# Performance work log

Hardware: AMD Instinct MI355X
Metric: run time of the kernel (lower is better)

Reference implementation:

```python
import jax, jax.numpy as jnp
import numpy as np
from jax import lax

IMG = 1280.0          # image side (80 * stride 16)
HF = WF = 80          # feature map
STRIDE = 16
A = 15                # anchors per location (5 sizes x 3 ratios)
KMIX = 5              # MDN mixture components
NIMG = 8
NGT = 32
PRE_NMS = 2000
POST_NMS = 1000
NMS_THRESH = 0.7
BATCH_PER_IMG = 256
POS_FRAC = 0.5
SCALE_CLAMP = float(np.log(1000.0 / 16.0))
LOG2PI = float(np.log(2.0 * np.pi))


def _make_anchors():
    sizes = np.array([32., 64., 128., 256., 512.])
    ratios = np.array([0.5, 1.0, 2.0])
    ws = (sizes[:, None] * np.sqrt(1.0 / ratios)[None, :]).reshape(-1)
    hs = (sizes[:, None] * np.sqrt(ratios)[None, :]).reshape(-1)
    base = np.stack([-ws / 2, -hs / 2, ws / 2, hs / 2], 1)  # [A,4]
    xs = (np.arange(WF) + 0.5) * STRIDE
    ys = (np.arange(HF) + 0.5) * STRIDE
    sx, sy = np.meshgrid(xs, ys)
    shifts = np.stack([sx.ravel(), sy.ravel(), sx.ravel(), sy.ravel()], 1)  # [HW,4]
    return jnp.asarray((shifts[:, None, :] + base[None]).reshape(-1, 4), jnp.float32)


def setup_inputs() -> dict:
    key = jax.random.key(0)
    k = jax.random.split(key, 6)
    R = HF * WF * A
    anchors = _make_anchors()                                                # [R,4]
    pi = jax.random.normal(k[0], (NIMG, KMIX, R), jnp.float32)
    mu = jax.random.normal(k[1], (NIMG, KMIX, R), jnp.float32)
    sigma = jax.random.uniform(k[2], (NIMG, KMIX, R), jnp.float32, 0.1, 1.0)
    deltas = jax.random.normal(k[3], (NIMG, R, 4), jnp.float32) * 0.1
    xy = jax.random.uniform(k[4], (NIMG, NGT, 2), jnp.float32, 0.0, 960.0)
    wh = jax.random.uniform(k[5], (NIMG, NGT, 2), jnp.float32, 20.0, 320.0)
    gt_boxes = jnp.concatenate([xy, xy + wh], -1)                            # [N,G,4]
    return {"anchors": anchors, "pi": pi, "mu": mu, "sigma": sigma,
            "deltas": deltas, "gt_boxes": gt_boxes}


def pairwise_iou(a, b):  # [M,4],[P,4] -> [M,P]
    area_a = (a[:, 2] - a[:, 0]) * (a[:, 3] - a[:, 1])
    area_b = (b[:, 2] - b[:, 0]) * (b[:, 3] - b[:, 1])
    lt = jnp.maximum(a[:, None, :2], b[None, :, :2])
    rb = jnp.minimum(a[:, None, 2:], b[None, :, 2:])
    wh = jnp.clip(rb - lt, 0.0)
    inter = wh[..., 0] * wh[..., 1]
    return inter / jnp.maximum(area_a[:, None] + area_b[None, :] - inter, 1e-9)


def apply_deltas(d, boxes):  # Box2BoxTransform.apply_deltas, weights=(1,1,1,1)
    w = boxes[:, 2] - boxes[:, 0]
    h = boxes[:, 3] - boxes[:, 1]
    cx = boxes[:, 0] + 0.5 * w
    cy = boxes[:, 1] + 0.5 * h
    dx, dy = d[:, 0], d[:, 1]
    dw = jnp.minimum(d[:, 2], SCALE_CLAMP)
    dh = jnp.minimum(d[:, 3], SCALE_CLAMP)
    pcx = dx * w + cx
    pcy = dy * h + cy
    pw = jnp.exp(dw) * w
    ph = jnp.exp(dh) * h
    return jnp.stack([pcx - 0.5 * pw, pcy - 0.5 * ph, pcx + 0.5 * pw, pcy + 0.5 * ph], 1)


def get_deltas(src, tgt):  # Box2BoxTransform.get_deltas
    sw = src[..., 2] - src[..., 0]
    sh = src[..., 3] - src[..., 1]
    scx = src[..., 0] + 0.5 * sw
    scy = src[..., 1] + 0.5 * sh
    tw = tgt[..., 2] - tgt[..., 0]
    th = tgt[..., 3] - tgt[..., 1]
    tcx = tgt[..., 0] + 0.5 * tw
    tcy = tgt[..., 1] + 0.5 * th
    return jnp.stack([(tcx - scx) / sw, (tcy - scy) / sh,
                      jnp.log(tw / sw), jnp.log(th / sh)], -1)


def _nms_image(boxes, scores, unc):  # [R,4],[R],[R,2] -> padded top proposals
    top_s, tidx = lax.top_k(scores, PRE_NMS)
    tb = jnp.clip(boxes[tidx], 0.0, IMG)   # clip to image
    tu = unc[tidx]
    iou = pairwise_iou(tb, tb)             # [PRE,PRE]
    ar = jnp.arange(PRE_NMS)

    def body(i, keep):
        sup = (iou[i] > NMS_THRESH) & (ar > i) & keep[i]
        return keep & ~sup

    keep = lax.fori_loop(0, PRE_NMS, body, jnp.ones((PRE_NMS,), bool))
    wv = tb[:, 2] - tb[:, 0]
    hv = tb[:, 3] - tb[:, 1]
    keep = keep & (wv > 0.0) & (hv > 0.0)  # min_box_size = 0
    ms = jnp.where(keep, top_s, -jnp.inf)
    out_s, oidx = lax.top_k(ms, POST_NMS)
    return tb[oidx], out_s, tu[oidx]


def _losses(anchors, pi, mu, sigma, deltas, gt_boxes):
    # label_and_sample_anchors (no_grad in torch)
    iou = lax.stop_gradient(jax.vmap(lambda g: pairwise_iou(g, anchors))(gt_boxes))  # [N,G,R]
    vals = iou.max(axis=1)                       # matched IoU quality  [N,R]
    idx = jnp.argmax(iou, axis=1)                # matched gt index     [N,R]
    labels = jnp.where(vals >= 0.7, 1, jnp.where(vals >= 0.3, -1, 0))
    best_gt = iou.max(axis=2)                    # [N,G]
    lq = jnp.any((iou >= best_gt[:, :, None] - 1e-7) & (best_gt[:, :, None] > 0), axis=1)
    labels = jnp.where(lq, 1, labels)            # allow_low_quality_matches
    # deterministic subsample to batch_size_per_image with positive_fraction
    pos = labels == 1
    neg = labels == 0
    n_pos = jnp.minimum(pos.sum(1), int(BATCH_PER_IMG * POS_FRAC))
    keep_pos = pos & (jnp.cumsum(pos, 1) <= n_pos[:, None])
    keep_neg = neg & (jnp.cumsum(neg, 1) <= (BATCH_PER_IMG - n_pos)[:, None])
    labels = jnp.where(keep_pos, 1, jnp.where(keep_neg, 0, -1))
    matched_gt = lax.stop_gradient(jax.vmap(lambda g, i: g[i])(gt_boxes, idx))  # [N,R,4]
    gt_deltas = get_deltas(lax.stop_gradient(anchors)[None], matched_gt)
    pos_mask = labels == 1
    # smooth_l1 with beta=0 -> L1, summed over positives
    loss_loc = jnp.sum(jnp.abs(deltas - gt_deltas) * pos_mask[..., None])
    valid = labels != -1
    t = jnp.clip(vals, 0.0, 1.0)
    lp = jax.nn.log_softmax(pi, axis=1)
    comp = lp - 0.5 * ((t[:, None, :] - mu) / sigma) ** 2 - jnp.log(sigma) - 0.5 * LOG2PI
    nll = -jax.nn.logsumexp(comp, axis=1)        # [N,R]
    loss_cls = jnp.sum(nll * valid)
    norm = BATCH_PER_IMG * pi.shape[0]
    return jnp.stack([loss_cls / norm, loss_loc / norm])


def reference(anchors, pi, mu, sigma, deltas, gt_boxes):
    # find_logit: pi-weighted mixture mean as objectness score
    pi_sm = jax.nn.softmax(pi, axis=1)           # [N,K,R]
    logits = jnp.sum(pi_sm * mu, axis=1)         # [N,R]
    # mdn_uncertainties: epistemic / aleatoric
    epis = jnp.sum(pi_sm * (mu - logits[:, None, :]) ** 2, axis=1)
    alea = jnp.sum(pi_sm * sigma ** 2, axis=1)
    unc = jnp.stack([epis, alea], -1)            # [N,R,2]
    # _decode_proposals
    boxes = jax.vmap(lambda d: apply_deltas(d, anchors))(deltas)  # [N,R,4]
    # find_top_rpn_proposals_uncertainty (pre-NMS topk, clip, NMS, post-NMS topk)
    prop_b, prop_s, prop_u = jax.vmap(_nms_image)(boxes, logits, unc)
    losses = _losses(anchors, pi, mu, sigma, deltas, gt_boxes)    # [loss_cls, loss_loc]
    return prop_b, prop_s, prop_u, losses
```

## Files before the change

### kernel.cpp

```cpp
#include <hip/hip_runtime.h>
#include <cstdint>
#include <cstddef>

typedef unsigned long long u64;
typedef unsigned int u32;
typedef unsigned short u16;
typedef unsigned char u8;

#define R_ANCH 96000
#define R4     24000
#define NIMG   8
#define KMIX   5
#define PRE    2000
#define POST   1000
#define NGT    32
#define NCHUNK 375
#define ACHUNK 94
#define NBLK   48
#define MROW   2048
#define SCAP   16
#define BIG_TH 64
#define CAP_BIN 6144
#define CAND_CAP 8192
#define GC_STRIDE 16
#define RPART  32

#define IMG_SZ        1280.0f
#define NMS_T         0.7f
#define SCALE_CLAMP_F 4.135166556742356f
#define HALF_L2PI     0.9189385332046727f

__device__ __forceinline__ u64 make_key(float s, int r) {
  u32 u = __float_as_uint(s);
  u = (u & 0x80000000u) ? ~u : (u | 0x80000000u);
  return ((u64)u << 32) | (u64)(0xFFFFFFFFu - (u32)r);
}

__device__ __forceinline__ float dec_score(u64 key) {
  u32 o = (u32)(key >> 32);
  u32 bits = (o & 0x80000000u) ? (o ^ 0x80000000u) : ~o;
  return __uint_as_float(bits);
}

__device__ __forceinline__ float iou_pair(float a0,float a1,float a2,float a3,
                                          float b0,float b1,float b2,float b3) {
#pragma clang fp contract(off)
  float areaA = (a2-a0)*(a3-a1);
  float areaB = (b2-b0)*(b3-b1);
  float lx=fmaxf(a0,b0), ly=fmaxf(a1,b1);
  float rx=fminf(a2,b2), ry=fminf(a3,b3);
  float iw=fmaxf(rx-lx,0.0f), ih=fmaxf(ry-ly,0.0f);
  float inter=iw*ih;
  return inter / fmaxf(areaA+areaB-inter, 1e-9f);
}

// ... 197 lines not shown
    int r = bx*256 + tid;
    if (tid < NGT*4) s_gt[tid] = gt[img*NGT*4 + tid];
    if (tid < NGT){
      const float* g4 = gt + img*NGT*4 + tid*4;
      s_ga[tid] = (g4[2]-g4[0])*(g4[3]-g4[1]);
      s_bg[tid] = __int_as_float(best[img*NGT + tid]);
    }
    __syncthreads();
    float4 a = ((const float4*)anchors)[r];
    float aA = (a.z-a.x)*(a.w-a.y);
    float bi=-1.0f, bu=1.0f; bool lq = false;
#pragma unroll 4
    for (int g=0; g<NGT; ++g){
      float g0=s_gt[g*4], g1=s_gt[g*4+1], g2=s_gt[g*4+2], g3=s_gt[g*4+3];
      float lx=fmaxf(g0,a.x), ly=fmaxf(g1,a.y);
      float rx=fminf(g2,a.z), ry=fminf(g3,a.w);
      float iw=fmaxf(rx-lx,0.0f), ih=fmaxf(ry-ly,0.0f);
      float inter=iw*ih;
      float uni = fmaxf(s_ga[g] + aA - inter, 1e-9f);
      if (inter*bu > bi*uni){ bi=inter; bu=uni; }
      float bg = s_bg[g];
      lq = lq || ((inter >= (bg - 1e-7f)*uni) && (bg > 0.0f));
    }
    float vbest = bi/bu;
    int lab = lq ? 1 : (vbest >= 0.7f ? 1 : (vbest >= 0.3f ? -1 : 0));
    label[(size_t)img*R_ANCH + r] = (signed char)lab;
    u64 bp = __ballot(lab==1), bn = __ballot(lab==0);
    int wid = tid>>6, lane = tid&63;
    if (lane==0){ s_w[wid*2]=__popcll(bp); s_w[wid*2+1]=__popcll(bn); }
    __syncthreads();
    if (tid==0){
      cpos[img*NCHUNK + bx] = s_w[0]+s_w[2]+s_w[4]+s_w[6];
      cneg[img*NCHUNK + bx] = s_w[1]+s_w[3]+s_w[5]+s_w[7];
    }
    return;
  }

  __shared__ u32 s_h[2048];
  __shared__ int s_i[8]; __shared__ u32 s_u[3];
  int d0,k0; u32 c0;
  pick2048(hist0 + img*2048, PRE, s_i, s_u, d0,k0,c0);
  if (c0 <= CAP_BIN) return;
  for (int b=tid; b<2048; b+=256) s_h[b]=0u;
  __syncthreads();
  const float* sc = logits + (size_t)img*R_ANCH;
  for (int r = blockIdx.x*256 + tid; r < R_ANCH; r += NBLK*256){
    u64 key = make_key(sc[r], r);
    if ((int)(key>>53) == d0) atomicAdd(&s_h[(u32)(key>>42)&2047u], 1u);
  }
  __syncthreads();
  for (int b=tid; b<2048; b+=256){ u32 v=s_h[b]; if(v) atomicAdd(&hist1[img*2048+b], v); }
}

__global__ __launch_bounds__(256) void kP2(const float* __restrict__ logits,
                                           const u32* __restrict__ hist0,
                                           const u32* __restrict__ hist1,
                                           u32* __restrict__ hist2) {
  __shared__ u32 s_h[2048];
  __shared__ int s_i[8]; __shared__ u32 s_u[3];
  int img = blockIdx.y, tid = threadIdx.x;
  int d0,k0; u32 c0;
  pick2048(hist0 + img*2048, PRE, s_i, s_u, d0,k0,c0);
  if (c0 <= CAP_BIN) return;
  int d1,k1; u32 c1;
  pick2048(hist1 + img*2048, k0, s_i, s_u, d1,k1,c1);
  if (c1 <= CAP_BIN) return;
  u64 p1 = ((u64)d0<<11) | (u64)d1;
  for (int b=tid; b<2048; b+=256) s_h[b]=0u;
  __syncthreads();
  const float* sc = logits + (size_t)img*R_ANCH;
  for (int r = blockIdx.x*256 + tid; r < R_ANCH; r += NBLK*256){
    u64 key = make_key(sc[r], r);
    if ((key>>42) == p1) atomicAdd(&s_h[(u32)(key>>31)&2047u], 1u);
  }
  __syncthreads();
  for (int b=tid; b<2048; b+=256){ u32 v=s_h[b]; if(v) atomicAdd(&hist2[img*2048+b], v); }
}

__global__ __launch_bounds__(256) void kGatherL4(const float* __restrict__ logits,
    const u32* __restrict__ hist0, const u32* __restrict__ hist1,
    const u32* __restrict__ hist2, u64* __restrict__ cand, u32* __restrict__ gcnt,
    const signed char* __restrict__ label,
    const float* __restrict__ pi, const float* __restrict__ mu,
    const float* __restrict__ sigma, const float* __restrict__ anchors,
    const float* __restrict__ gt, const float* __restrict__ deltas,
    const int* __restrict__ cpos, const int* __restrict__ cneg,
    float* __restrict__ acc) {
  int img = blockIdx.y, tid = threadIdx.x;

  if (blockIdx.x >= NBLK) {
    __shared__ int s_wp[4], s_wn[4];
    __shared__ int s_r[12];
    __shared__ float s_red[8];
    __shared__ float s_gt[NGT*4];
    int bx = blockIdx.x - NBLK;
    int lane = tid & 63, wid = tid >> 6;
    if (tid < NGT*4) s_gt[tid] = gt[img*NGT*4 + tid];
    int vp=0, vn=0, tp=0;
    for (int k=tid; k<NCHUNK; k+=256){
      int cp = cpos[img*NCHUNK + k];
      int cn = cneg[img*NCHUNK + k];
      tp += cp;
      if (k < bx){ vp += cp; vn += cn; }
    }
    for (int of=32; of>0; of>>=1){
      vp += __shfl_down(vp, of, 64);
      vn += __shfl_down(vn, of, 64);
      tp += __shfl_down(tp, of, 64);
    }
    if (lane==0){ s_r[wid]=vp; s_r[4+wid]=vn; s_r[8+wid]=tp; }
    __syncthreads();
    int pre_p = s_r[0]+s_r[1]+s_r[2]+s_r[3];
    int pre_n = s_r[4]+s_r[5]+s_r[6]+s_r[7];
    int totp  = s_r[8]+s_r[9]+s_r[10]+s_r[11];
    int np = totp < 128 ? totp : 128;
    int nn = 256 - np;
    int r = bx*256 + tid;
    size_t o = (size_t)img*R_ANCH + r;
    int lab = label[o];
    bool pos = (lab==1), neg = (lab==0);
    u64 bp = __ballot(pos), bn = __ballot(neg);
    if (lane==0){ s_wp[wid]=__popcll(bp); s_wn[wid]=__popcll(bn); }
    __syncthreads();
    for (int w=0; w<wid; ++w){ pre_p += s_wp[w]; pre_n += s_wn[w]; }
    u64 lm = (1ull<<lane) - 1ull;
    pre_p += __popcll(bp & lm);
    pre_n += __popcll(bn & lm);
    bool kp = pos && (pre_p < np);
    bool kn = neg && (pre_n < nn);
    float c_cls = 0.0f, c_loc = 0.0f;
    if (kp || kn){
      float4 a = ((const float4*)anchors)[r];
      float aA = (a.z-a.x)*(a.w-a.y);
      float bi = -1.0f, bu = 1.0f; int idx = 0;
// ... 16 lines not shown
        p[k]=pi[base+(size_t)k*R_ANCH];
        m[k]=mu[base+(size_t)k*R_ANCH];
        s[k]=sigma[base+(size_t)k*R_ANCH];
      }
      float mx = p[0];
#pragma unroll
      for (int k=1;k<KMIX;k++) mx = fmaxf(mx,p[k]);
      float e[KMIX]; float sum = 0.0f;
#pragma unroll
      for (int k=0;k<KMIX;k++){ e[k]=expf(p[k]-mx); sum += e[k]; }
      float lsum = logf(sum);
      float t_ = fminf(fmaxf(vbest, 0.0f), 1.0f);
      float comp[KMIX];
#pragma unroll
      for (int k=0;k<KMIX;k++){
        float z = (t_ - m[k]) / s[k];
        comp[k] = (p[k]-mx-lsum) - 0.5f*z*z - logf(s[k]) - HALF_L2PI;
      }
      float cm = comp[0];
#pragma unroll
      for (int k=1;k<KMIX;k++) cm = fmaxf(cm, comp[k]);
      float se = 0.0f;
#pragma unroll
      for (int k=0;k<KMIX;k++) se += expf(comp[k]-cm);
      c_cls = -(cm + logf(se));
      if (kp){
        const float* gb = &s_gt[idx*4];
        float sw = a.z-a.x, sh = a.w-a.y;
        float scx = a.x+0.5f*sw, scy = a.y+0.5f*sh;
        float tw = gb[2]-gb[0], th = gb[3]-gb[1];
        float tcx = gb[0]+0.5f*tw, tcy = gb[1]+0.5f*th;
        float4 d = ((const float4*)deltas)[(size_t)img*R_ANCH + r];
        c_loc = fabsf(d.x-(tcx-scx)/sw) + fabsf(d.y-(tcy-scy)/sh)
              + fabsf(d.z-logf(tw/sw)) + fabsf(d.w-logf(th/sh));
      }
    }
    for (int of=32; of>0; of>>=1){
      c_cls += __shfl_down(c_cls, of, 64);
      c_loc += __shfl_down(c_loc, of, 64);
    }
    if (lane==0){ s_red[wid]=c_cls; s_red[4+wid]=c_loc; }
    __syncthreads();
    if (tid==0){
      float a = s_red[0]+s_red[1]+s_red[2]+s_red[3];
      float b = s_red[4]+s_red[5]+s_red[6]+s_red[7];
      if (a != 0.0f) atomicAdd(&acc[0], a);
      if (b != 0.0f) atomicAdd(&acc[1], b);
    }
    return;
  }

  __shared__ int s_i[8]; __shared__ u32 s_u[3];
  __shared__ u64 s_cand[2048];
  __shared__ u32 s_cnt, s_base;
  if (tid==0) s_cnt = 0u;
  int d,kk; u32 c;
  pick2048(hist0 + img*2048, PRE, s_i, s_u, d,kk,c);
  u64 p = (u64)d; int L = 0;
  if (c > CAP_BIN){
    pick2048(hist1 + img*2048, kk, s_i, s_u, d,kk,c);
    p = (p<<11)|(u64)d; L = 1;
    if (c > CAP_BIN){
      pick2048(hist2 + img*2048, kk, s_i, s_u, d,kk,c);
      p = (p<<11)|(u64)d; L = 2;
    }
  }
  u64 T = p << (64 - 11*(L+1));
  const float* sc = logits + (size_t)img*R_ANCH;
  int lane = tid & 63;
  for (int r = blockIdx.x*256 + tid; r < R_ANCH; r += NBLK*256){
    u64 key = make_key(sc[r], r);
    bool take = (key >= T);
    u64 b = __ballot(take);
    if (b){
      u32 base = 0;
      if (lane==0) base = atomicAdd(&s_cnt, (u32)__popcll(b));
      base = (u32)__shfl((int)base, 0, 64);
      if (take){
        u32 pos = base + (u32)__popcll(b & ((1ull<<lane)-1ull));
        if (pos < 2048u) s_cand[pos] = key;
        else {
          u32 gp = atomicAdd(&gcnt[img*GC_STRIDE], 1u);
          if (gp < CAND_CAP) cand[(size_t)img*CAND_CAP + gp] = key;
        }
      }
    }
  }
  __syncthreads();
  u32 n = s_cnt < 2048u ? s_cnt : 2048u;
  if (tid==0) s_base = atomicAdd(&gcnt[img*GC_STRIDE], n);
  __syncthreads();
  u32 gb = s_base;
  for (u32 i=tid; i<n; i+=256)
    cand[(size_t)img*CAND_CAP + gb + i] = s_cand[i];
}

__global__ __launch_bounds__(1024) void kRank(
    const u64* __restrict__ cand, const u32* __restrict__ gcnt,
    const float* __restrict__ epis, const float* __restrict__ alea,
    const float* __restrict__ deltas, const float* __restrict__ anchors,
    float* __restrict__ tb, float* __restrict__ tu, float* __restrict__ ts) {
  __shared__ u64 s_key[CAND_CAP];
  __shared__ u16 s_idx0[CAND_CAP];
  __shared__ u16 s_idx1[CAND_CAP];
  __shared__ u32 s_h0[2048];
  __shared__ u32 s_off0[2048];
  __shared__ u32 s_h1[2048];
  __shared__ u32 s_off1[2048];
  __shared__ u32 s_wsum[16];
  __shared__ u32 s_nbig;
  __shared__ u16 s_big[128];
  int tid = threadIdx.x, part = blockIdx.x, img = blockIdx.y;
  u32 cnt = gcnt[img*GC_STRIDE];
  if (cnt > (u32)CAND_CAP) cnt = CAND_CAP;
  const u64* cp = cand + (size_t)img*CAND_CAP;
  for (int i=tid; i<CAND_CAP; i+=1024) s_key[i] = (i < (int)cnt) ? cp[i] : 0ull;
  for (int b=tid; b<2048; b+=1024){ s_h0[b] = 0u; }
  if (tid==0) s_nbig = 0u;
  __syncthreads();
  for (int i=tid; i<(int)cnt; i+=1024)
    atomicAdd(&s_h0[(u32)(s_key[i]>>53)], 1u);
  __syncthreads();
  scan2048_desc(s_h0, s_off0, s_wsum, tid);
  __syncthreads();
  for (int b=tid; b<2048; b+=1024){
    u32 sz = s_h0[b];
    if (sz > BIG_TH && s_off0[b] < PRE && (b % RPART) == part){
      u32 q = atomicAdd(&s_nbig, 1u);
      if (q < 128u) s_big[q] = (u16)b;
    }
  }
  __syncthreads();
  for (int i=tid; i<(int)cnt; i+=1024){
    u32 d = (u32)(s_key[i]>>53);
    u32 slot = atomicAdd(&s_off0[d], 1u);
    s_idx0[slot] = (u16)i;
  }
  __syncthreads();
  auto emit = [&](u64 my, u32 rank){
    if (rank < PRE){
      int p = (int)rank;
      u32 idx = 0xFFFFFFFFu - (u32)(my & 0xFFFFFFFFull);
      ts[img*PRE + p] = dec_score(my);
      float4 a = ((const float4*)anchors)[idx];
      float4 dd = ((const float4*)deltas)[(size_t)img*R_ANCH + idx];
      float w = a.z - a.x, h = a.w - a.y;
      float cx = a.x + 0.5f*w, cy = a.y + 0.5f*h;
      float dw = fminf(dd.z, SCALE_CLAMP_F), dh = fminf(dd.w, SCALE_CLAMP_F);
      float pcx = dd.x*w + cx, pcy = dd.y*h + cy;
      float pw = expf(dw)*w, ph = expf(dh)*h;
      float x0 = fminf(fmaxf(pcx - 0.5f*pw, 0.0f), IMG_SZ);
      float y0 = fminf(fmaxf(pcy - 0.5f*ph, 0.0f), IMG_SZ);
      float x1 = fminf(fmaxf(pcx + 0.5f*pw, 0.0f), IMG_SZ);
      float y1 = fminf(fmaxf(pcy + 0.5f*ph, 0.0f), IMG_SZ);
      ((float4*)tb)[(size_t)img*PRE + p] = make_float4(x0,y0,x1,y1);
      size_t o = (size_t)img*R_ANCH + idx;
      ((float2*)tu)[(size_t)img*PRE + p] = make_float2(epis[o], alea[o]);
    }
  };
  {
    int lo = (int)(((long long)cnt * part) / RPART);
    int hi = (int)(((long long)cnt * (part+1)) / RPART);
    for (int i=lo+tid; i<hi; i+=1024){
      u64 my = s_key[i];
      u32 d = (u32)(my>>53);
      u32 size = s_h0[d];
      if (size > BIG_TH) continue;
      u32 bs = s_off0[d] - size;
      if (bs >= PRE) continue;
      u32 rank = bs;
      for (u32 q=bs; q<bs+size; ++q)
        rank += (s_key[s_idx0[q]] > my) ? 1u : 0u;
      emit(my, rank);
    }
  }
  __syncthreads();
  u32 nbig = s_nbig < 128u ? s_nbig : 128u;
  for (u32 bb=0; bb<nbig; ++bb){
    u32 B = s_big[bb];
    u32 size = s_h0[B];
    u32 base0 = s_off0[B] - size;
    for (int b=tid; b<2048; b+=1024) s_h1[b] = 0u;
    __syncthreads();
    for (u32 q=tid; q<size; q+=1024){
      u64 k = s_key[s_idx0[base0+q]];
      atomicAdd(&s_h1[(u32)(k>>42)&2047u], 1u);
    }
    __syncthreads();
    scan2048_desc(s_h1, s_off1, s_wsum, tid);
    __syncthreads();
    for (u32 q=tid; q<size; q+=1024){
      u16 ci = s_idx0[base0+q];
      u64 k = s_key[ci];
      u32 slot = atomicAdd(&s_off1[(u32)(k>>42)&2047u], 1u);
      s_idx1[slot] = ci;
    }
    __syncthreads();
    for (u32 q=tid; q<size; q+=1024){
      u16 ci = s_idx1[q];
      u64 my = s_key[ci];
      u32 d1 = (u32)(my>>42)&2047u;
      u32 ssz = s_h1[d1];
      u32 sbs = s_off1[d1] - ssz;
      u32 rank = base0 + sbs;
      for (u32 t2=sbs; t2<sbs+ssz; ++t2)
        rank += (s_key[s_idx1[t2]] > my) ? 1u : 0u;
      emit(my, rank);
    }
    __syncthreads();
  }
}

__global__ __launch_bounds__(1024) void kD_mask(const float* __restrict__ tb,
                                                u64* __restrict__ maskLT,
                                                u32* __restrict__ scnt,
                                                u16* __restrict__ slist) {
  __shared__ float4 s_tile[64];
  int tid = threadIdx.x;
  int a = blockIdx.x, img = blockIdx.y;
  const float4* tbi = (const float4*)tb + (size_t)img*PRE;
  if (tid < 64){
    int i = a*64 + tid;
    s_tile[tid] = (i < PRE) ? tbi[i] : make_float4(0.f,0.f,0.f,0.f);
  }
  __syncthreads();
  u64* outp = maskLT + ((size_t)img*32 + a)*MROW;
  u32* cnts = scnt + (size_t)img*2048;
  u16* lst  = slist + (size_t)img*2048*SCAP;
  int bmax = min(64, PRE - a*64);
  for (int j = a*64 + tid; j < MROW; j += 1024){
    u64 m = 0ull;
    if (j < PRE){
      float4 B = tbi[j];
      int blim = min(bmax, j - a*64);
      for (int b = 0; b < blim; ++b){
        float4 A = s_tile[b];
        float v = iou_pair(A.x,A.y,A.z,A.w, B.x,B.y,B.z,B.w);
        m |= (u64)(v > NMS_T) << b;
      }
    }
    outp[j] = m;
    u64 mm = m;
    while (mm){
      int b = __builtin_ctzll(mm); mm &= mm - 1ull;
      u32 slot = atomicAdd(&cnts[j], 1u);
      if (slot < SCAP) lst[(size_t)j*SCAP + slot] = (u16)(a*64 + b);
    }
  }
}

__global__ __launch_bounds__(1024) void kEF_nms(const u64* __restrict__ maskLT,
    const u32* __restrict__ scnt, const u16* __restrict__ slist,
    const float* __restrict__ tb, const float* __restrict__ tu,
    const float* __restrict__ ts, const float* __restrict__ acc,
    float* __restrict__ out) {
  __shared__ u64 s_list64[2048*SCAP/4];
  __shared__ u16 s_cnt[2048];
  __shared__ u8  kbuf[2][2048];
  __shared__ u64 s_kw[32];
  __shared__ int s_change, s_ovf;
  __shared__ int s_wk[16], s_wn[16];
  __shared__ int s_kc, s_runk, s_runn;
  int img = blockIdx.x, tid = threadIdx.x;
  int lane = tid & 63, wid = tid >> 6;
  const u64* gl = (const u64*)(slist + (size_t)img*2048*SCAP);
  for (int i=tid; i<2048*SCAP/4; i+=1024) s_list64[i] = gl[i];
  const u32* gc = scnt + (size_t)img*2048;
  for (int i=tid; i<2048; i+=1024) s_cnt[i] = (u16)gc[i];
  if (tid==0){ s_change = 0; s_ovf = 0; }
  __syncthreads();
  bool myovf = false;
#pragma unroll
  for (int q=0; q<2; ++q){
    int j = tid + q*1024;
    if (s_cnt[j] > SCAP) myovf = true;
    kbuf[0][j] = (j < PRE) ? 1 : 0;
  }
  if (myovf) s_ovf = 1;
  __syncthreads();
  const u64* MT = maskLT + (size_t)img*32*MROW;
  int cur = 0;
  for (int iter=0; iter<2048; ++iter){
    bool ovf = (s_ovf != 0);
    if (ovf && tid < 32){
      u64 w = 0ull;
      for (int b=0; b<64; ++b) w |= (u64)(kbuf[cur][tid*64+b] & 1) << b;
      s_kw[tid] = w;
    }
    __syncthreads();
    bool changed = false;
#pragma unroll
    for (int q=0; q<2; ++q){
      int j = tid + q*1024;
      u8 old = kbuf[cur][j];
      u8 nk = (j < PRE) ? 1 : 0;
      if (nk){
        int cnt = s_cnt[j];
        if (cnt <= SCAP){
          const u16* lp = (const u16*)&s_list64[j*(SCAP/4)];
          for (int i=0; i<cnt; ++i){
            if (kbuf[cur][lp[i]]){ nk = 0; break; }
          }
        } else {
          int amax = j >> 6;
          for (int a=0; a<=amax; ++a){
            if (MT[(size_t)a*MROW + j] & s_kw[a]){ nk = 0; break; }
          }
        }
      }
      kbuf[1-cur][j] = nk;
      changed |= (nk != old);
    }
    if (changed) s_change = 1;
    __syncthreads();
    int ch = s_change;
    __syncthreads();
    if (tid==0) s_change = 0;
    if (!ch) break;
    cur ^= 1;
  }
  __syncthreads();
  const float4* tbi = (const float4*)tb + (size_t)img*PRE;
  const float NEG_INF = __uint_as_float(0xff800000u);
  u8* kf = kbuf[1-cur];
#pragma unroll
  for (int cch=0; cch<2; ++cch){
    int pp = cch*1024 + tid;
    bool kp = false;
    if (pp < PRE && kbuf[cur][pp]){
      float4 b = tbi[pp];
      kp = (b.z > b.x) && (b.w > b.y);
    }
    kf[pp] = kp ? 1 : 0;
  }
  __syncthreads();
  {
    int cc = (int)kf[tid] + (int)kf[1024 + tid];
    for (int of=32; of>0; of>>=1) cc += __shfl_down(cc, of, 64);
    if (lane==0) s_wk[wid] = cc;
  }
  __syncthreads();
  if (tid==0){
    int t=0; for (int w=0; w<16; ++w) t += s_wk[w];
    s_kc = t; s_runk = 0; s_runn = 0;
  }
  __syncthreads();
  int kc = s_kc;
#pragma unroll
  for (int cch=0; cch<2; ++cch){
    int pp = cch*1024 + tid;
    bool kp = kf[pp] != 0;
    u64 bk = __ballot(kp), bn = __ballot(!kp);
    if (lane==0){ s_wk[wid]=__popcll(bk); s_wn[wid]=__popcll(bn); }
    __syncthreads();
    int pk = s_runk, pn = s_runn;
    for (int w=0; w<wid; ++w){ pk += s_wk[w]; pn += s_wn[w]; }
    u64 lm = (1ull<<lane) - 1ull;
    pk += __popcll(bk & lm);
    pn += __popcll(bn & lm);
    int slot = kp ? pk : (kc + pn);
    if (slot < POST && pp < PRE){
      ((float4*)out)[img*POST + slot] = tbi[pp];
      out[32000 + img*POST + slot] = kp ? ts[img*PRE + pp] : NEG_INF;
      ((float2*)(out + 40000))[img*POST + slot] = ((const float2*)tu)[(size_t)img*PRE + pp];
    }
    __syncthreads();
    if (tid==0){
      int tk=0, tn=0;
      for (int w=0; w<16; ++w){ tk += s_wk[w]; tn += s_wn[w]; }
      s_runk += tk; s_runn += tn;
    }
    __syncthreads();
  }
  if (img==0 && tid<2) out[56000+tid] = acc[tid] * (1.0f/2048.0f);
}

extern "C" void kernel_launch(void* const* d_in, const int* in_sizes, int n_in,
                              void* d_out, int out_size, void* d_ws, size_t ws_size,
                              hipStream_t stream) {
  const float* anchors = (const float*)d_in[0];
  const float* pi      = (const float*)d_in[1];
  const float* mu      = (const float*)d_in[2];
  const float* sigma   = (const float*)d_in[3];
  const float* deltas  = (const float*)d_in[4];
  const float* gt      = (const float*)d_in[5];
  float* out = (float*)d_out;

  char* ws = (char*)d_ws;
  size_t off = 0;
  auto alloc = [&](size_t bytes) -> void* {
    void* p = (void*)(ws + off);
    off += (bytes + 255) & ~(size_t)255;
    return p;
  };
  float* logits = (float*)alloc((size_t)NIMG*R_ANCH*4);
  float* epis   = (float*)alloc((size_t)NIMG*R_ANCH*4);
  float* alea   = (float*)alloc((size_t)NIMG*R_ANCH*4);
  signed char* label = (signed char*)alloc((size_t)NIMG*R_ANCH);
  float* tb     = (float*)alloc((size_t)NIMG*PRE*4*4);
  float* tu     = (float*)alloc((size_t)NIMG*PRE*2*4);
  float* ts     = (float*)alloc((size_t)NIMG*PRE*4);
  u64*   maskLT = (u64*)  alloc((size_t)NIMG*32*MROW*8);
  u16*   slist  = (u16*)  alloc((size_t)NIMG*2048*SCAP*2);
  u64*   cand   = (u64*)  alloc((size_t)NIMG*CAND_CAP*8);
  int*   cpos   = (int*)  alloc((size_t)NIMG*NCHUNK*4);
  int*   cneg   = (int*)  alloc((size_t)NIMG*NCHUNK*4);
  size_t zstart = off;
  u32*   hist0  = (u32*)  alloc((size_t)NIMG*2048*4);
  u32*   hist1  = (u32*)  alloc((size_t)NIMG*2048*4);
  u32*   hist2  = (u32*)  alloc((size_t)NIMG*2048*4);
  u32*   gcnt   = (u32*)  alloc((size_t)NIMG*GC_STRIDE*4);
  int*   best   = (int*)  alloc((size_t)NIMG*NGT*4);
  u32*   scnt   = (u32*)  alloc((size_t)NIMG*2048*4);
  float* acc    = (float*)alloc(8);
  int zwords = (int)((off - zstart) / 4);

  kZero<<<dim3(64), dim3(256), 0, stream>>>((u32*)(ws + zstart), zwords);
  kA_mdn<<<dim3(ACHUNK+NBLK, NIMG), dim3(256), 0, stream>>>(pi, mu, sigma, logits, epis, alea,
                                                            hist0, anchors, gt, best);
  kP1L2<<<dim3(NBLK+NCHUNK, NIMG), dim3(256), 0, stream>>>(logits, hist0, hist1,
                                                           anchors, gt, best, label, cpos, cneg);
  kP2<<<dim3(NBLK, NIMG), dim3(256), 0, stream>>>(logits, hist0, hist1, hist2);
  kGatherL4<<<dim3(NBLK+NCHUNK, NIMG), dim3(256), 0, stream>>>(logits, hist0, hist1, hist2,
                                                               cand, gcnt, label, pi, mu, sigma,
                                                               anchors, gt, deltas, cpos, cneg, acc);
  kRank<<<dim3(RPART, NIMG), dim3(1024), 0, stream>>>(cand, gcnt, epis, alea, deltas, anchors, tb, tu, ts);
  kD_mask<<<dim3(32, NIMG), dim3(1024), 0, stream>>>(tb, maskLT, scnt, slist);
  kEF_nms<<<dim3(NIMG), dim3(1024), 0, stream>>>(maskLT, scnt, slist, tb, tu, ts, acc, out);
}
```

Before: 239.3 us.

## Fuse rank, NMS-mask and NMS kernels into one cooperative kernel; drop kP2

Rank, IoU-mask build and NMS selection now run in one cooperatively launched kernel. Phases are separated by grid-wide syncs, and shared memory is reused through a union. The separate level-2 histogram kernel is removed: when a third radix level is needed, each gather block builds that histogram redundantly in its own shared memory. This cuts two kernel launches and their inter-kernel gaps. In exchange it adds grid-sync cost, requires all blocks to be co-resident, and makes every gather block rescan the full logit array when the rare level-2 case triggers.

```diff
diff --git a/kernel.cpp b/kernel.cpp
--- a/kernel.cpp
+++ b/kernel.cpp
@@ -1,6 +1,9 @@
 #include <hip/hip_runtime.h>
+#include <hip/hip_cooperative_groups.h>
 #include <cstdint>
 #include <cstddef>
+
+namespace cg = cooperative_groups;
 
 typedef unsigned long long u64;
 typedef unsigned int u32;
@@ -304,34 +307,9 @@
   for (int b=tid; b<2048; b+=256){ u32 v=s_h[b]; if(v) atomicAdd(&hist1[img*2048+b], v); }
 }
 
-__global__ __launch_bounds__(256) void kP2(const float* __restrict__ logits,
-                                           const u32* __restrict__ hist0,
-                                           const u32* __restrict__ hist1,
-                                           u32* __restrict__ hist2) {
-  __shared__ u32 s_h[2048];
-  __shared__ int s_i[8]; __shared__ u32 s_u[3];
-  int img = blockIdx.y, tid = threadIdx.x;
-  int d0,k0; u32 c0;
-  pick2048(hist0 + img*2048, PRE, s_i, s_u, d0,k0,c0);
-  if (c0 <= CAP_BIN) return;
-  int d1,k1; u32 c1;
-  pick2048(hist1 + img*2048, k0, s_i, s_u, d1,k1,c1);
-  if (c1 <= CAP_BIN) return;
-  u64 p1 = ((u64)d0<<11) | (u64)d1;
-  for (int b=tid; b<2048; b+=256) s_h[b]=0u;
-  __syncthreads();
-  const float* sc = logits + (size_t)img*R_ANCH;
-  for (int r = blockIdx.x*256 + tid; r < R_ANCH; r += NBLK*256){
-    u64 key = make_key(sc[r], r);
-    if ((key>>42) == p1) atomicAdd(&s_h[(u32)(key>>31)&2047u], 1u);
-  }
-  __syncthreads();
-  for (int b=tid; b<2048; b+=256){ u32 v=s_h[b]; if(v) atomicAdd(&hist2[img*2048+b], v); }
-}
-
 __global__ __launch_bounds__(256) void kGatherL4(const float* __restrict__ logits,
     const u32* __restrict__ hist0, const u32* __restrict__ hist1,
-    const u32* __restrict__ hist2, u64* __restrict__ cand, u32* __restrict__ gcnt,
+    u64* __restrict__ cand, u32* __restrict__ gcnt,
     const signed char* __restrict__ label,
     const float* __restrict__ pi, const float* __restrict__ mu,
     const float* __restrict__ sigma, const float* __restrict__ anchors,
@@ -454,21 +432,29 @@
 
   __shared__ int s_i[8]; __shared__ u32 s_u[3];
   __shared__ u64 s_cand[2048];
+  __shared__ u32 s_h2[2048];
   __shared__ u32 s_cnt, s_base;
   if (tid==0) s_cnt = 0u;
   int d,kk; u32 c;
   pick2048(hist0 + img*2048, PRE, s_i, s_u, d,kk,c);
   u64 p = (u64)d; int L = 0;
+  const float* sc = logits + (size_t)img*R_ANCH;
   if (c > CAP_BIN){
     pick2048(hist1 + img*2048, kk, s_i, s_u, d,kk,c);
     p = (p<<11)|(u64)d; L = 1;
     if (c > CAP_BIN){
-      pick2048(hist2 + img*2048, kk, s_i, s_u, d,kk,c);
+      for (int b=tid; b<2048; b+=256) s_h2[b] = 0u;
+      __syncthreads();
+      for (int r = tid; r < R_ANCH; r += 256){
+        u64 key = make_key(sc[r], r);
+        if ((key>>42) == p) atomicAdd(&s_h2[(u32)(key>>31)&2047u], 1u);
+      }
+      __syncthreads();
+      pick2048(s_h2, kk, s_i, s_u, d,kk,c);
       p = (p<<11)|(u64)d; L = 2;
     }
   }
   u64 T = p << (64 - 11*(L+1));
-  const float* sc = logits + (size_t)img*R_ANCH;
   int lane = tid & 63;
   for (int r = blockIdx.x*256 + tid; r < R_ANCH; r += NBLK*256){
     u64 key = make_key(sc[r], r);
@@ -497,284 +483,293 @@
     cand[(size_t)img*CAND_CAP + gb + i] = s_cand[i];
 }
 
-__global__ __launch_bounds__(1024) void kRank(
+struct RankS {
+  u64 s_key[CAND_CAP];
+  u16 s_idx0[CAND_CAP];
+  u16 s_idx1[CAND_CAP];
+  u32 s_h0[2048];
+  u32 s_off0[2048];
+  u32 s_h1[2048];
+  u32 s_off1[2048];
+  u32 s_wsum[16];
+  u32 s_nbig;
+  u16 s_big[128];
+};
+struct DmaskS { float4 s_tile[64]; };
+struct EfS {
+  u64 s_list64[2048*SCAP/4];
+  u16 s_cnt[2048];
+  u8  kbuf[2][2048];
+  u64 s_kw[32];
+  int s_change, s_ovf;
+  int s_wk[16], s_wn[16];
+  int s_kc, s_runk, s_runn;
+};
+
+__global__ __launch_bounds__(1024) void kRDE(
     const u64* __restrict__ cand, const u32* __restrict__ gcnt,
     const float* __restrict__ epis, const float* __restrict__ alea,
     const float* __restrict__ deltas, const float* __restrict__ anchors,
-    float* __restrict__ tb, float* __restrict__ tu, float* __restrict__ ts) {
-  __shared__ u64 s_key[CAND_CAP];
-  __shared__ u16 s_idx0[CAND_CAP];
-  __shared__ u16 s_idx1[CAND_CAP];
-  __shared__ u32 s_h0[2048];
-  __shared__ u32 s_off0[2048];
-  __shared__ u32 s_h1[2048];
-  __shared__ u32 s_off1[2048];
-  __shared__ u32 s_wsum[16];
-  __shared__ u32 s_nbig;
-  __shared__ u16 s_big[128];
-  int tid = threadIdx.x, part = blockIdx.x, img = blockIdx.y;
-  u32 cnt = gcnt[img*GC_STRIDE];
-  if (cnt > (u32)CAND_CAP) cnt = CAND_CAP;
-  const u64* cp = cand + (size_t)img*CAND_CAP;
-  for (int i=tid; i<CAND_CAP; i+=1024) s_key[i] = (i < (int)cnt) ? cp[i] : 0ull;
-  for (int b=tid; b<2048; b+=1024){ s_h0[b] = 0u; }
-  if (tid==0) s_nbig = 0u;
-  __syncthreads();
-  for (int i=tid; i<(int)cnt; i+=1024)
-    atomicAdd(&s_h0[(u32)(s_key[i]>>53)], 1u);
-  __syncthreads();
-  scan2048_desc(s_h0, s_off0, s_wsum, tid);
-  __syncthreads();
-  for (int b=tid; b<2048; b+=1024){
-    u32 sz = s_h0[b];
-    if (sz > BIG_TH && s_off0[b] < PRE && (b % RPART) == part){
-      u32 q = atomicAdd(&s_nbig, 1u);
-      if (q < 128u) s_big[q] = (u16)b;
-    }
-  }
-  __syncthreads();
-  for (int i=tid; i<(int)cnt; i+=1024){
-    u32 d = (u32)(s_key[i]>>53);
-    u32 slot = atomicAdd(&s_off0[d], 1u);
-    s_idx0[slot] = (u16)i;
-  }
-  __syncthreads();
-  auto emit = [&](u64 my, u32 rank){
-    if (rank < PRE){
-      int p = (int)rank;
-      u32 idx = 0xFFFFFFFFu - (u32)(my & 0xFFFFFFFFull);
-      ts[img*PRE + p] = dec_score(my);
-      float4 a = ((const float4*)anchors)[idx];
-      float4 dd = ((const float4*)deltas)[(size_t)img*R_ANCH + idx];
-      float w = a.z - a.x, h = a.w - a.y;
-      float cx = a.x + 0.5f*w, cy = a.y + 0.5f*h;
-      float dw = fminf(dd.z, SCALE_CLAMP_F), dh = fminf(dd.w, SCALE_CLAMP_F);
-      float pcx = dd.x*w + cx, pcy = dd.y*h + cy;
-      float pw = expf(dw)*w, ph = expf(dh)*h;
-      float x0 = fminf(fmaxf(pcx - 0.5f*pw, 0.0f), IMG_SZ);
-      float y0 = fminf(fmaxf(pcy - 0.5f*ph, 0.0f), IMG_SZ);
-      float x1 = fminf(fmaxf(pcx + 0.5f*pw, 0.0f), IMG_SZ);
-      float y1 = fminf(fmaxf(pcy + 0.5f*ph, 0.0f), IMG_SZ);
-      ((float4*)tb)[(size_t)img*PRE + p] = make_float4(x0,y0,x1,y1);
-      size_t o = (size_t)img*R_ANCH + idx;
-      ((float2*)tu)[(size_t)img*PRE + p] = make_float2(epis[o], alea[o]);
-    }
-  };
+    float* __restrict__ tb, float* __restrict__ tu, float* __restrict__ ts,
+    u64* __restrict__ maskLT, u32* __restrict__ scnt, u16* __restrict__ slist,
+    const float* __restrict__ acc, float* __restrict__ out) {
+  __shared__ union { RankS r; DmaskS d; EfS e; } sm;
+  cg::grid_group grid = cg::this_grid();
+  int tid = threadIdx.x;
+  int gblk = blockIdx.x;
+
   {
-    int lo = (int)(((long long)cnt * part) / RPART);
-    int hi = (int)(((long long)cnt * (part+1)) / RPART);
-    for (int i=lo+tid; i<hi; i+=1024){
-      u64 my = s_key[i];
-      u32 d = (u32)(my>>53);
-      u32 size = s_h0[d];
-      if (size > BIG_TH) continue;
-      u32 bs = s_off0[d] - size;
-      if (bs >= PRE) continue;
-      u32 rank = bs;
-      for (u32 q=bs; q<bs+size; ++q)
-        rank += (s_key[s_idx0[q]] > my) ? 1u : 0u;
-      emit(my, rank);
-    }
-  }
-  __syncthreads();
-  u32 nbig = s_nbig < 128u ? s_nbig : 128u;
-  for (u32 bb=0; bb<nbig; ++bb){
-    u32 B = s_big[bb];
-    u32 size = s_h0[B];
-    u32 base0 = s_off0[B] - size;
-    for (int b=tid; b<2048; b+=1024) s_h1[b] = 0u;
-    __syncthreads();
-    for (u32 q=tid; q<size; q+=1024){
-      u64 k = s_key[s_idx0[base0+q]];
-      atomicAdd(&s_h1[(u32)(k>>42)&2047u], 1u);
-    }
-    __syncthreads();
-    scan2048_desc(s_h1, s_off1, s_wsum, tid);
-    __syncthreads();
-    for (u32 q=tid; q<size; q+=1024){
-      u16 ci = s_idx0[base0+q];
-      u64 k = s_key[ci];
-      u32 slot = atomicAdd(&s_off1[(u32)(k>>42)&2047u], 1u);
-      s_idx1[slot] = ci;
-    }
-    __syncthreads();
-    for (u32 q=tid; q<size; q+=1024){
-      u16 ci = s_idx1[q];
-      u64 my = s_key[ci];
-      u32 d1 = (u32)(my>>42)&2047u;
-      u32 ssz = s_h1[d1];
-      u32 sbs = s_off1[d1] - ssz;
-      u32 rank = base0 + sbs;
-      for (u32 t2=sbs; t2<sbs+ssz; ++t2)
-        rank += (s_key[s_idx1[t2]] > my) ? 1u : 0u;
-      emit(my, rank);
-    }
-    __syncthreads();
-  }
-}
-
-__global__ __launch_bounds__(1024) void kD_mask(const float* __restrict__ tb,
-                                                u64* __restrict__ maskLT,
-                                                u32* __restrict__ scnt,
-                                                u16* __restrict__ slist) {
-  __shared__ float4 s_tile[64];
-  int tid = threadIdx.x;
-  int a = blockIdx.x, img = blockIdx.y;
-  const float4* tbi = (const float4*)tb + (size_t)img*PRE;
-  if (tid < 64){
-    int i = a*64 + tid;
-    s_tile[tid] = (i < PRE) ? tbi[i] : make_float4(0.f,0.f,0.f,0.f);
-  }
-  __syncthreads();
-  u64* outp = maskLT + ((size_t)img*32 + a)*MROW;
-  u32* cnts = scnt + (size_t)img*2048;
-  u16* lst  = slist + (size_t)img*2048*SCAP;
-  int bmax = min(64, PRE - a*64);
-  for (int j = a*64 + tid; j < MROW; j += 1024){
-    u64 m = 0ull;
-    if (j < PRE){
-      float4 B = tbi[j];
-      int blim = min(bmax, j - a*64);
-      for (int b = 0; b < blim; ++b){
-        float4 A = s_tile[b];
-        float v = iou_pair(A.x,A.y,A.z,A.w, B.x,B.y,B.z,B.w);
-        m |= (u64)(v > NMS_T) << b;
-      }
-    }
-    outp[j] = m;
-    u64 mm = m;
-    while (mm){
-      int b = __builtin_ctzll(mm); mm &= mm - 1ull;
-      u32 slot = atomicAdd(&cnts[j], 1u);
-      if (slot < SCAP) lst[(size_t)j*SCAP + slot] = (u16)(a*64 + b);
-    }
-  }
-}
-
-__global__ __launch_bounds__(1024) void kEF_nms(const u64* __restrict__ maskLT,
-    const u32* __restrict__ scnt, const u16* __restrict__ slist,
-    const float* __restrict__ tb, const float* __restrict__ tu,
-    const float* __restrict__ ts, const float* __restrict__ acc,
-    float* __restrict__ out) {
-  __shared__ u64 s_list64[2048*SCAP/4];
-  __shared__ u16 s_cnt[2048];
-  __shared__ u8  kbuf[2][2048];
-  __shared__ u64 s_kw[32];
-  __shared__ int s_change, s_ovf;
-  __shared__ int s_wk[16], s_wn[16];
-  __shared__ int s_kc, s_runk, s_runn;
-  int img = blockIdx.x, tid = threadIdx.x;
-  int lane = tid & 63, wid = tid >> 6;
-  const u64* gl = (const u64*)(slist + (size_t)img*2048*SCAP);
-  for (int i=tid; i<2048*SCAP/4; i+=1024) s_list64[i] = gl[i];
-  const u32* gc = scnt + (size_t)img*2048;
-  for (int i=tid; i<2048; i+=1024) s_cnt[i] = (u16)gc[i];
-  if (tid==0){ s_change = 0; s_ovf = 0; }
-  __syncthreads();
-  bool myovf = false;
-#pragma unroll
-  for (int q=0; q<2; ++q){
-    int j = tid + q*1024;
-    if (s_cnt[j] > SCAP) myovf = true;
-    kbuf[0][j] = (j < PRE) ? 1 : 0;
-  }
-  if (myovf) s_ovf = 1;
-  __syncthreads();
-  const u64* MT = maskLT + (size_t)img*32*MROW;
-  int cur = 0;
-  for (int iter=0; iter<2048; ++iter){
-    bool ovf = (s_ovf != 0);
-    if (ovf && tid < 32){
-      u64 w = 0ull;
-      for (int b=0; b<64; ++b) w |= (u64)(kbuf[cur][tid*64+b] & 1) << b;
-      s_kw[tid] = w;
-    }
-    __syncthreads();
-    bool changed = false;
+    int part = gblk & (RPART-1), img = gblk / RPART;
+    u32 cnt = gcnt[img*GC_STRIDE];
+    if (cnt > (u32)CAND_CAP) cnt = CAND_CAP;
+    const u64* cp = cand + (size_t)img*CAND_CAP;
+    for (int i=tid; i<CAND_CAP; i+=1024) sm.r.s_key[i] = (i < (int)cnt) ? cp[i] : 0ull;
+    for (int b=tid; b<2048; b+=1024){ sm.r.s_h0[b] = 0u; }
+    if (tid==0) sm.r.s_nbig = 0u;
+    __syncthreads();
+    for (int i=tid; i<(int)cnt; i+=1024)
+      atomicAdd(&sm.r.s_h0[(u32)(sm.r.s_key[i]>>53)], 1u);
+    __syncthreads();
+    scan2048_desc(sm.r.s_h0, sm.r.s_off0, sm.r.s_wsum, tid);
+    __syncthreads();
+    for (int b=tid; b<2048; b+=1024){
+      u32 sz = sm.r.s_h0[b];
+      if (sz > BIG_TH && sm.r.s_off0[b] < PRE && (b % RPART) == part){
+        u32 q = atomicAdd(&sm.r.s_nbig, 1u);
+        if (q < 128u) sm.r.s_big[q] = (u16)b;
+      }
+    }
+    __syncthreads();
+    for (int i=tid; i<(int)cnt; i+=1024){
+      u32 d = (u32)(sm.r.s_key[i]>>53);
+      u32 slot = atomicAdd(&sm.r.s_off0[d], 1u);
+      sm.r.s_idx0[slot] = (u16)i;
+    }
+    __syncthreads();
+    auto emit = [&](u64 my, u32 rank){
+      if (rank < PRE){
+        int p = (int)rank;
+        u32 idx = 0xFFFFFFFFu - (u32)(my & 0xFFFFFFFFull);
+        ts[img*PRE + p] = dec_score(my);
+        float4 a = ((const float4*)anchors)[idx];
+        float4 dd = ((const float4*)deltas)[(size_t)img*R_ANCH + idx];
+        float w = a.z - a.x, h = a.w - a.y;
+        float cx = a.x + 0.5f*w, cy = a.y + 0.5f*h;
+        float dw = fminf(dd.z, SCALE_CLAMP_F), dh = fminf(dd.w, SCALE_CLAMP_F);
+        float pcx = dd.x*w + cx, pcy = dd.y*h + cy;
+        float pw = expf(dw)*w, ph = expf(dh)*h;
+        float x0 = fminf(fmaxf(pcx - 0.5f*pw, 0.0f), IMG_SZ);
+        float y0 = fminf(fmaxf(pcy - 0.5f*ph, 0.0f), IMG_SZ);
+        float x1 = fminf(fmaxf(pcx + 0.5f*pw, 0.0f), IMG_SZ);
+        float y1 = fminf(fmaxf(pcy + 0.5f*ph, 0.0f), IMG_SZ);
+        ((float4*)tb)[(size_t)img*PRE + p] = make_float4(x0,y0,x1,y1);
+        size_t o = (size_t)img*R_ANCH + idx;
+        ((float2*)tu)[(size_t)img*PRE + p] = make_float2(epis[o], alea[o]);
+      }
+    };
+    {
+      int lo = (int)(((long long)cnt * part) / RPART);
+      int hi = (int)(((long long)cnt * (part+1)) / RPART);
+      for (int i=lo+tid; i<hi; i+=1024){
+        u64 my = sm.r.s_key[i];
+        u32 d = (u32)(my>>53);
+        u32 size = sm.r.s_h0[d];
+        if (size > BIG_TH) continue;
+        u32 bs = sm.r.s_off0[d] - size;
+        if (bs >= PRE) continue;
+        u32 rank = bs;
+        for (u32 q=bs; q<bs+size; ++q)
+          rank += (sm.r.s_key[sm.r.s_idx0[q]] > my) ? 1u : 0u;
+        emit(my, rank);
+      }
+    }
+    __syncthreads();
+    u32 nbig = sm.r.s_nbig < 128u ? sm.r.s_nbig : 128u;
+    for (u32 bb=0; bb<nbig; ++bb){
+      u32 B = sm.r.s_big[bb];
+      u32 size = sm.r.s_h0[B];
+      u32 base0 = sm.r.s_off0[B] - size;
+      for (int b=tid; b<2048; b+=1024) sm.r.s_h1[b] = 0u;
+      __syncthreads();
+      for (u32 q=tid; q<size; q+=1024){
+        u64 k = sm.r.s_key[sm.r.s_idx0[base0+q]];
+        atomicAdd(&sm.r.s_h1[(u32)(k>>42)&2047u], 1u);
+      }
+      __syncthreads();
+      scan2048_desc(sm.r.s_h1, sm.r.s_off1, sm.r.s_wsum, tid);
+      __syncthreads();
+      for (u32 q=tid; q<size; q+=1024){
+        u16 ci = sm.r.s_idx0[base0+q];
+        u64 k = sm.r.s_key[ci];
+        u32 slot = atomicAdd(&sm.r.s_off1[(u32)(k>>42)&2047u], 1u);
+        sm.r.s_idx1[slot] = ci;
+      }
+      __syncthreads();
+      for (u32 q=tid; q<size; q+=1024){
+        u16 ci = sm.r.s_idx1[q];
+        u64 my = sm.r.s_key[ci];
+        u32 d1 = (u32)(my>>42)&2047u;
+        u32 ssz = sm.r.s_h1[d1];
+        u32 sbs = sm.r.s_off1[d1] - ssz;
+        u32 rank = base0 + sbs;
+        for (u32 t2=sbs; t2<sbs+ssz; ++t2)
+          rank += (sm.r.s_key[sm.r.s_idx1[t2]] > my) ? 1u : 0u;
+        emit(my, rank);
+      }
+      __syncthreads();
+    }
+  }
+  grid.sync();
+
+  {
+    int a = gblk & 31, img = gblk >> 5;
+    const float4* tbi = (const float4*)tb + (size_t)img*PRE;
+    if (tid < 64){
+      int i = a*64 + tid;
+      sm.d.s_tile[tid] = (i < PRE) ? tbi[i] : make_float4(0.f,0.f,0.f,0.f);
+    }
+    __syncthreads();
+    u64* outp = maskLT + ((size_t)img*32 + a)*MROW;
+    u32* cnts = scnt + (size_t)img*2048;
+    u16* lst  = slist + (size_t)img*2048*SCAP;
+    int bmax = min(64, PRE - a*64);
+    for (int j = a*64 + tid; j < MROW; j += 1024){
+      u64 m = 0ull;
+      if (j < PRE){
+        float4 B = tbi[j];
+        int blim = min(bmax, j - a*64);
+        for (int b = 0; b < blim; ++b){
+          float4 A = sm.d.s_tile[b];
+          float v = iou_pair(A.x,A.y,A.z,A.w, B.x,B.y,B.z,B.w);
+          m |= (u64)(v > NMS_T) << b;
+        }
+      }
+      outp[j] = m;
+      u64 mm = m;
+      while (mm){
+        int b = __builtin_ctzll(mm); mm &= mm - 1ull;
+        u32 slot = atomicAdd(&cnts[j], 1u);
+        if (slot < SCAP) lst[(size_t)j*SCAP + slot] = (u16)(a*64 + b);
+      }
+    }
+  }
+  grid.sync();
+
+  if (gblk >= NIMG) return;
+  {
+    int img = gblk;
+    int lane = tid & 63, wid = tid >> 6;
+    const u64* gl = (const u64*)(slist + (size_t)img*2048*SCAP);
+    for (int i=tid; i<2048*SCAP/4; i+=1024) sm.e.s_list64[i] = gl[i];
+    const u32* gc = scnt + (size_t)img*2048;
+    for (int i=tid; i<2048; i+=1024) sm.e.s_cnt[i] = (u16)gc[i];
+    if (tid==0){ sm.e.s_change = 0; sm.e.s_ovf = 0; }
+    __syncthreads();
+    bool myovf = false;
 #pragma unroll
     for (int q=0; q<2; ++q){
       int j = tid + q*1024;
-      u8 old = kbuf[cur][j];
-      u8 nk = (j < PRE) ? 1 : 0;
-      if (nk){
-        int cnt = s_cnt[j];
-        if (cnt <= SCAP){
-          const u16* lp = (const u16*)&s_list64[j*(SCAP/4)];
-          for (int i=0; i<cnt; ++i){
-            if (kbuf[cur][lp[i]]){ nk = 0; break; }
-          }
-        } else {
-          int amax = j >> 6;
-          for (int a=0; a<=amax; ++a){
-            if (MT[(size_t)a*MROW + j] & s_kw[a]){ nk = 0; break; }
+      if (sm.e.s_cnt[j] > SCAP) myovf = true;
+      sm.e.kbuf[0][j] = (j < PRE) ? 1 : 0;
+    }
+    if (myovf) sm.e.s_ovf = 1;
+    __syncthreads();
+    const u64* MT = maskLT + (size_t)img*32*MROW;
+    int cur = 0;
+    for (int iter=0; iter<2048; ++iter){
+      bool ovf = (sm.e.s_ovf != 0);
+      if (ovf && tid < 32){
+        u64 w = 0ull;
+        for (int b=0; b<64; ++b) w |= (u64)(sm.e.kbuf[cur][tid*64+b] & 1) << b;
+        sm.e.s_kw[tid] = w;
+      }
+      __syncthreads();
+      bool changed = false;
+#pragma unroll
+      for (int q=0; q<2; ++q){
+        int j = tid + q*1024;
+        u8 old = sm.e.kbuf[cur][j];
+        u8 nk = (j < PRE) ? 1 : 0;
+        if (nk){
+          int cnt = sm.e.s_cnt[j];
+          if (cnt <= SCAP){
+            const u16* lp = (const u16*)&sm.e.s_list64[j*(SCAP/4)];
+            for (int i=0; i<cnt; ++i){
+              if (sm.e.kbuf[cur][lp[i]]){ nk = 0; break; }
+            }
+          } else {
+            int amax = j >> 6;
+            for (int a=0; a<=amax; ++a){
+              if (MT[(size_t)a*MROW + j] & sm.e.s_kw[a]){ nk = 0; break; }
+            }
           }
         }
-      }
-      kbuf[1-cur][j] = nk;
-      changed |= (nk != old);
-    }
-    if (changed) s_change = 1;
-    __syncthreads();
-    int ch = s_change;
-    __syncthreads();
-    if (tid==0) s_change = 0;
-    if (!ch) break;
-    cur ^= 1;
-  }
-  __syncthreads();
-  const float4* tbi = (const float4*)tb + (size_t)img*PRE;
-  const float NEG_INF = __uint_as_float(0xff800000u);
-  u8* kf = kbuf[1-cur];
-#pragma unroll
-  for (int cch=0; cch<2; ++cch){
-    int pp = cch*1024 + tid;
-    bool kp = false;
-    if (pp < PRE && kbuf[cur][pp]){
-      float4 b = tbi[pp];
-      kp = (b.z > b.x) && (b.w > b.y);
-    }
-    kf[pp] = kp ? 1 : 0;
-  }
-  __syncthreads();
-  {
-    int cc = (int)kf[tid] + (int)kf[1024 + tid];
-    for (int of=32; of>0; of>>=1) cc += __shfl_down(cc, of, 64);
-    if (lane==0) s_wk[wid] = cc;
-  }
-  __syncthreads();
-  if (tid==0){
-    int t=0; for (int w=0; w<16; ++w) t += s_wk[w];
-    s_kc = t; s_runk = 0; s_runn = 0;
-  }
-  __syncthreads();
-  int kc = s_kc;
-#pragma unroll
-  for (int cch=0; cch<2; ++cch){
-    int pp = cch*1024 + tid;
-    bool kp = kf[pp] != 0;
-    u64 bk = __ballot(kp), bn = __ballot(!kp);
-    if (lane==0){ s_wk[wid]=__popcll(bk); s_wn[wid]=__popcll(bn); }
-    __syncthreads();
-    int pk = s_runk, pn = s_runn;
-    for (int w=0; w<wid; ++w){ pk += s_wk[w]; pn += s_wn[w]; }
-    u64 lm = (1ull<<lane) - 1ull;
-    pk += __popcll(bk & lm);
-    pn += __popcll(bn & lm);
-    int slot = kp ? pk : (kc + pn);
-    if (slot < POST && pp < PRE){
-      ((float4*)out)[img*POST + slot] = tbi[pp];
-      out[32000 + img*POST + slot] = kp ? ts[img*PRE + pp] : NEG_INF;
-      ((float2*)(out + 40000))[img*POST + slot] = ((const float2*)tu)[(size_t)img*PRE + pp];
+        sm.e.kbuf[1-cur][j] = nk;
+        changed |= (nk != old);
+      }
+      if (changed) sm.e.s_change = 1;
+      __syncthreads();
+      int ch = sm.e.s_change;
+      __syncthreads();
+      if (tid==0) sm.e.s_change = 0;
+      if (!ch) break;
+      cur ^= 1;
+    }
+    __syncthreads();
+    const float4* tbi = (const float4*)tb + (size_t)img*PRE;
+    const float NEG_INF = __uint_as_float(0xff800000u);
+    u8* kf = sm.e.kbuf[1-cur];
+#pragma unroll
+    for (int cch=0; cch<2; ++cch){
+      int pp = cch*1024 + tid;
+      bool kp = false;
+      if (pp < PRE && sm.e.kbuf[cur][pp]){
+        float4 b = tbi[pp];
+        kp = (b.z > b.x) && (b.w > b.y);
+      }
+      kf[pp] = kp ? 1 : 0;
+    }
+    __syncthreads();
+    {
+      int cc = (int)kf[tid] + (int)kf[1024 + tid];
+      for (int of=32; of>0; of>>=1) cc += __shfl_down(cc, of, 64);
+      if (lane==0) sm.e.s_wk[wid] = cc;
     }
     __syncthreads();
     if (tid==0){
-      int tk=0, tn=0;
-      for (int w=0; w<16; ++w){ tk += s_wk[w]; tn += s_wn[w]; }
-      s_runk += tk; s_runn += tn;
-    }
-    __syncthreads();
-  }
-  if (img==0 && tid<2) out[56000+tid] = acc[tid] * (1.0f/2048.0f);
+      int t=0; for (int w=0; w<16; ++w) t += sm.e.s_wk[w];
+      sm.e.s_kc = t; sm.e.s_runk = 0; sm.e.s_runn = 0;
+    }
+    __syncthreads();
+    int kc = sm.e.s_kc;
+#pragma unroll
+    for (int cch=0; cch<2; ++cch){
+      int pp = cch*1024 + tid;
+      bool kp = kf[pp] != 0;
+      u64 bk = __ballot(kp), bn = __ballot(!kp);
+      if (lane==0){ sm.e.s_wk[wid]=__popcll(bk); sm.e.s_wn[wid]=__popcll(bn); }
+      __syncthreads();
+      int pk = sm.e.s_runk, pn = sm.e.s_runn;
+      for (int w=0; w<wid; ++w){ pk += sm.e.s_wk[w]; pn += sm.e.s_wn[w]; }
+      u64 lm = (1ull<<lane) - 1ull;
+      pk += __popcll(bk & lm);
+      pn += __popcll(bn & lm);
+      int slot = kp ? pk : (kc + pn);
+      if (slot < POST && pp < PRE){
+        ((float4*)out)[img*POST + slot] = tbi[pp];
+        out[32000 + img*POST + slot] = kp ? ts[img*PRE + pp] : NEG_INF;
+        ((float2*)(out + 40000))[img*POST + slot] = ((const float2*)tu)[(size_t)img*PRE + pp];
+      }
+      __syncthreads();
+      if (tid==0){
+        int tk=0, tn=0;
+        for (int w=0; w<16; ++w){ tk += sm.e.s_wk[w]; tn += sm.e.s_wn[w]; }
+        sm.e.s_runk += tk; sm.e.s_runn += tn;
+      }
+      __syncthreads();
+    }
+    if (img==0 && tid<2) out[56000+tid] = acc[tid] * (1.0f/2048.0f);
+  }
 }
 
 extern "C" void kernel_launch(void* const* d_in, const int* in_sizes, int n_in,
@@ -810,7 +805,6 @@
   size_t zstart = off;
   u32*   hist0  = (u32*)  alloc((size_t)NIMG*2048*4);
   u32*   hist1  = (u32*)  alloc((size_t)NIMG*2048*4);
-  u32*   hist2  = (u32*)  alloc((size_t)NIMG*2048*4);
   u32*   gcnt   = (u32*)  alloc((size_t)NIMG*GC_STRIDE*4);
   int*   best   = (int*)  alloc((size_t)NIMG*NGT*4);
   u32*   scnt   = (u32*)  alloc((size_t)NIMG*2048*4);
@@ -822,11 +816,19 @@
                                                             hist0, anchors, gt, best);
   kP1L2<<<dim3(NBLK+NCHUNK, NIMG), dim3(256), 0, stream>>>(logits, hist0, hist1,
                                                            anchors, gt, best, label, cpos, cneg);
-  kP2<<<dim3(NBLK, NIMG), dim3(256), 0, stream>>>(logits, hist0, hist1, hist2);
-  kGatherL4<<<dim3(NBLK+NCHUNK, NIMG), dim3(256), 0, stream>>>(logits, hist0, hist1, hist2,
+  kGatherL4<<<dim3(NBLK+NCHUNK, NIMG), dim3(256), 0, stream>>>(logits, hist0, hist1,
                                                                cand, gcnt, label, pi, mu, sigma,
                                                                anchors, gt, deltas, cpos, cneg, acc);
-  kRank<<<dim3(RPART, NIMG), dim3(1024), 0, stream>>>(cand, gcnt, epis, alea, deltas, anchors, tb, tu, ts);
-  kD_mask<<<dim3(32, NIMG), dim3(1024), 0, stream>>>(tb, maskLT, scnt, slist);
-  kEF_nms<<<dim3(NIMG), dim3(1024), 0, stream>>>(maskLT, scnt, slist, tb, tu, ts, acc, out);
-}
+  {
+    const u64* cand_c = cand; const u32* gcnt_c = gcnt;
+    const float* epis_c = epis; const float* alea_c = alea;
+    const float* acc_c = acc;
+    void* kargs[] = {
+      (void*)&cand_c, (void*)&gcnt_c, (void*)&epis_c, (void*)&alea_c,
+      (void*)&deltas, (void*)&anchors, (void*)&tb, (void*)&tu, (void*)&ts,
+      (void*)&maskLT, (void*)&scnt, (void*)&slist, (void*)&acc_c, (void*)&out
+    };
+    hipLaunchCooperativeKernel(reinterpret_cast<void*>(kRDE),
+                               dim3(RPART*NIMG), dim3(1024), kargs, 0, stream);
+  }
+}
```

Measured after the change: 292.0 us. +22.0%, slower.
